# Kernel tuning notes

Measured on AMD Instinct MI355X. Metric: run time of the kernel, lower is better.

The kernel has to match this reference:

```python
import jax, jax.numpy as jnp
import numpy as np

H = 2  # attention heads (n_heads)


def _time_enc(t, tw, tb):
    # TGN TimeEncode: cos(t * w + b); t [...,] -> [..., T]
    return jnp.cos(t[..., None] * tw + tb)


def _level0(nodes, node_features, memory_tab):
    # memory[src] + node_features[src]
    return memory_tab[nodes] + node_features[nodes]


def _aggregate(l, src_feat, src_te, neigh, ete, efeat, mask,
               Wq, bq, Wk, bk, Wv, bv, Wo, bo, fc1_w, fc1_b, fc2_w, fc2_b):
    # Temporal graph attention (TGN TemporalAttentionLayer) with padding mask.
    N, K, _ = neigh.shape
    Dq = Wq.shape[-1]
    dh = Dq // H
    q_in = jnp.concatenate([src_feat[:, None, :], src_te], axis=-1)   # [N,1,Dq]
    k_in = jnp.concatenate([neigh, ete, efeat], axis=-1)              # [N,K,Dk]
    q = (q_in @ Wq[l] + bq[l]).reshape(N, 1, H, dh)
    k = (k_in @ Wk[l] + bk[l]).reshape(N, K, H, dh)
    v = (k_in @ Wv[l] + bv[l]).reshape(N, K, H, dh)
    scores = jnp.einsum('nqhd,nkhd->nhqk', q, k) / jnp.sqrt(jnp.asarray(dh, q.dtype))
    all_masked = mask.all(axis=-1)                                    # [N]
    # TGN trick: un-mask column 0 for fully-masked rows, zero output later
    eff_mask = mask & ~(all_masked[:, None] & (jnp.arange(K) == 0))
    scores = jnp.where(eff_mask[:, None, None, :], -1e9, scores)
    attn = jax.nn.softmax(scores, axis=-1)
    o = jnp.einsum('nhqk,nkhd->nqhd', attn, v).reshape(N, Dq)
    o = o @ Wo[l] + bo[l]
    o = jnp.where(all_masked[:, None], 0.0, o)
    # MergeLayer: fc2(relu(fc1(cat[attn_out, src_feat])))
    h = jax.nn.relu(jnp.concatenate([o, src_feat], axis=-1) @ fc1_w[l] + fc1_b[l])
    return h @ fc2_w[l] + fc2_b[l]


def setup_inputs() -> dict:
    key = jax.random.key(0)
    ks = jax.random.split(key, 24)
    B, K, Nn, Ne, D, T = 2048, 20, 1_000_000, 1_000_000, 128, 128
    Dq, Dk = D + T, D + T + D
    inp = {}
    inp['node_features'] = jax.random.normal(ks[0], (Nn, D), jnp.float32) * 0.1
    inp['edge_feat_table'] = jax.random.normal(ks[1], (Ne, D), jnp.float32) * 0.1
    inp['memory_tab'] = jax.random.normal(ks[2], (Nn, D), jnp.float32) * 0.1
    inp['timestamps'] = jax.random.uniform(ks[3], (B,), jnp.float32) * 100.0
    inp['etimes_src'] = jax.random.uniform(ks[4], (B, K), jnp.float32) * 100.0
    inp['etimes_nbr'] = jax.random.uniform(ks[5], (B * K, K), jnp.float32) * 100.0
    inp['tw'] = jax.random.normal(ks[6], (T,), jnp.float32)
    inp['tb'] = jax.random.normal(ks[7], (T,), jnp.float32)
    inp['Wq'] = jax.random.normal(ks[8], (2, Dq, Dq), jnp.float32) / np.sqrt(Dq)
    inp['bq'] = jnp.zeros((2, Dq), jnp.float32)
    inp['Wk'] = jax.random.normal(ks[9], (2, Dk, Dq), jnp.float32) / np.sqrt(Dk)
    inp['bk'] = jnp.zeros((2, Dq), jnp.float32)
    inp['Wv'] = jax.random.normal(ks[10], (2, Dk, Dq), jnp.float32) / np.sqrt(Dk)
    inp['bv'] = jnp.zeros((2, Dq), jnp.float32)
    inp['Wo'] = jax.random.normal(ks[11], (2, Dq, Dq), jnp.float32) / np.sqrt(Dq)
    inp['bo'] = jnp.zeros((2, Dq), jnp.float32)
    inp['fc1_w'] = jax.random.normal(ks[12], (2, Dq + D, D), jnp.float32) / np.sqrt(Dq + D)
    inp['fc1_b'] = jnp.zeros((2, D), jnp.float32)
    inp['fc2_w'] = jax.random.normal(ks[13], (2, D, D), jnp.float32) / np.sqrt(D)
    inp['fc2_b'] = jnp.zeros((2, D), jnp.float32)
    inp['source_nodes'] = jax.random.randint(ks[14], (B,), 0, Nn)
    inp['nbrs_src'] = jax.random.randint(ks[15], (B, K), 0, Nn)
    inp['eidx_src'] = jax.random.randint(ks[16], (B, K), 0, Ne)
    inp['nbrs_nbr'] = jax.random.randint(ks[17], (B * K, K), 0, Nn)
    inp['eidx_nbr'] = jax.random.randint(ks[18], (B * K, K), 0, Ne)
    return inp


def reference(node_features, edge_feat_table, memory_tab, timestamps,
              etimes_src, etimes_nbr, tw, tb,
              Wq, bq, Wk, bk, Wv, bv, Wo, bo, fc1_w, fc1_b, fc2_w, fc2_b,
              source_nodes, nbrs_src, eidx_src, nbrs_nbr, eidx_nbr):
    B, K = nbrs_src.shape
    D = node_features.shape[-1]
    params = (Wq, bq, Wk, bk, Wv, bv, Wo, bo, fc1_w, fc1_b, fc2_w, fc2_b)

    def layer1(nodes, ts, nbrs, eidx, etimes):
        # one temporal-attention hop (n_layers == 1 recursion level)
        src = _level0(nodes, node_features, memory_tab)                 # [N,D]
        neigh = _level0(nbrs.reshape(-1), node_features, memory_tab).reshape(*nbrs.shape, D)
        ete = _time_enc(ts[:, None] - etimes, tw, tb)                   # [N,K,T]
        src_te = _time_enc(jnp.zeros((nodes.shape[0], 1), ts.dtype), tw, tb)
        efeat = edge_feat_table[eidx]                                   # [N,K,De]
        mask = nbrs == 0
        return _aggregate(0, src, src_te, neigh, ete, efeat, mask, *params)

    # layer-1 embedding of sources (recursion uses same temporal neighbors)
    src_conv = layer1(source_nodes, timestamps, nbrs_src, eidx_src, etimes_src)  # [B,D]
    # layer-1 embedding of the sources' neighbors
    ts_rep = jnp.repeat(timestamps, K)                                  # [B*K]
    neigh_emb = layer1(nbrs_src.reshape(-1), ts_rep, nbrs_nbr, eidx_nbr, etimes_nbr)
    neigh_emb = neigh_emb.reshape(B, K, D)
    # layer-2 aggregation over the sources' neighbors
    ete = _time_enc(timestamps[:, None] - etimes_src, tw, tb)           # [B,K,T]
    src_te = _time_enc(jnp.zeros((B, 1), timestamps.dtype), tw, tb)
    efeat = edge_feat_table[eidx_src]
    mask = nbrs_src == 0
    return _aggregate(1, src_conv, src_te, neigh_emb, ete, efeat, mask, *params)
```

## Files before the change

kernel.cpp:

```cpp
#include <hip/hip_runtime.h>
#include <hip/hip_bf16.h>

#define NB   2048
#define KN   20
#define DF   128
#define DQ   256
#define DKI  384
#define NR1  43008
#define SCALE 0.08838834764831845f

typedef short s16x8 __attribute__((ext_vector_type(8)));
typedef short s16x4 __attribute__((ext_vector_type(4)));
typedef float f32x4 __attribute__((ext_vector_type(4)));

__device__ __hip_bfloat16 g_S   [(size_t)NR1*128];
__device__ __hip_bfloat16 g_QKH [(size_t)NR1*768];
__device__ __hip_bfloat16 g_CTX [(size_t)NR1*768];
__device__ __hip_bfloat16 g_Ob  [(size_t)NR1*256];
__device__ __hip_bfloat16 g_FC1A[(size_t)NR1*384];
__device__ float          g_out1[(size_t)NR1*DF];
__device__ float          g_Wqk [2*256*768];
__device__ float          g_bqk [2*768];
__device__ float          g_bqkv[2*768];
__device__ unsigned char  g_allm[NR1];
__device__ __hip_bfloat16 g_Bqk[2*98304];
__device__ __hip_bfloat16 g_Bv [4*49152];
__device__ __hip_bfloat16 g_Bo [2*65536];
__device__ __hip_bfloat16 g_B1 [2*49152];
__device__ __hip_bfloat16 g_B2 [2*16384];

__device__ __forceinline__ short f2bf(float v) {
  union { __hip_bfloat16 h; short s; } u; u.h = __float2bfloat16(v); return u.s;
}
__device__ __forceinline__ float2 bfpair(unsigned u) {
  union { unsigned u2; float f; } a, b;
  a.u2 = u << 16;
  b.u2 = u & 0xFFFF0000u;
  float2 r; r.x = a.f; r.y = b.f; return r;
}
__device__ __forceinline__ s16x4 pack4(float x, float y, float z, float w) {
  s16x4 o; o[0]=f2bf(x); o[1]=f2bf(y); o[2]=f2bf(z); o[3]=f2bf(w); return o;
}
__device__ __forceinline__ unsigned packbf2(float2 v) {
  return (unsigned)(unsigned short)f2bf(v.x) | ((unsigned)(unsigned short)f2bf(v.y) << 16);
}

__global__ __launch_bounds__(256)
void k_wprep1(const float* __restrict__ Wq, const float* __restrict__ Wk,
              const float* __restrict__ bq, const float* __restrict__ Wv,
              const float* __restrict__ Wo, const float* __restrict__ f1w,
              const float* __restrict__ f2w) {
  int b = blockIdx.x;
  if (b < 1536) {
    int idx = b*256 + threadIdx.x;
    int L = idx / 196608, rem = idx % 196608;
    int n = rem >> 8, co = rem & 255;
    int h = n / 384, i = n - h*384;
    const float* wqp = Wq + (size_t)L*DQ*DQ  + (size_t)co*DQ + h*128;
    const float* wkp = Wk + (size_t)L*DKI*DQ + (size_t)i*DQ  + h*128;
    float acc = 0.f;
    #pragma unroll 4
    for (int c = 0; c < 128; ++c) acc += wqp[c]*wkp[c];
    g_Wqk[(size_t)(L*256 + co)*768 + n] = acc;
    if (co == 0) {
      const float* bqp = bq + L*DQ + h*128;
      float bb = 0.f;
      for (int c = 0; c < 128; ++c) bb += bqp[c]*wkp[c];
      g_bqk[L*768 + n] = bb;
    }
    return;
  }
  b -= 1536;
  const float* src; int ldsrc, K, N; __hip_bfloat16* dst;
  if (b < 96)       { int j = b/24; int L=j>>1, h=j&1;
                      src = Wv + (size_t)L*DKI*DQ + h*128; ldsrc=256; K=384; N=128;
                      dst = g_Bv + (size_t)j*49152; b %= 24; }
  else if (b < 160) { b -= 96; int L = b/32;
                      src = Wo + (size_t)L*DQ*DQ; ldsrc=256; K=256; N=256;
                      dst = g_Bo + (size_t)L*65536; b %= 32; }
  else if (b < 208) { b -= 160; int L = b/24;
                      src = f1w + (size_t)L*384*128; ldsrc=128; K=384; N=128;
                      dst = g_B1 + (size_t)L*49152; b %= 24; }
  else              { b -= 208; int L = b/8;
                      src = f2w + (size_t)L*128*128; ldsrc=128; K=128; N=128;
                      dst = g_B2 + (size_t)L*16384; b %= 8; }
  int slot = b*256 + threadIdx.x;
  if (slot >= (K*N)/8) return;
  int cl = slot & 15, t = slot >> 4;
  int kgn = K >> 3;
  int kg = t % kgn, nt = t / kgn;
  int n = nt*16 + cl;
  s16x8 o;
  #pragma unroll
  for (int e = 0; e < 8; ++e) o[e] = f2bf(src[(size_t)(kg*8 + e)*ldsrc + n]);
  *(s16x8*)(dst + (size_t)slot*8) = o;
}

__global__ __launch_bounds__(256)
void k_wprep2(const float* __restrict__ tb) {
  int b = blockIdx.x;
  if (b < 96) {
    int L = b / 48;
    int slot = (b % 48)*256 + threadIdx.x;
    int cl = slot & 15, t = slot >> 4;
    int kg = t & 15, nt = t >> 4;
    int n = nt*16 + cl;
    s16x8 o;
    #pragma unroll
    for (int e = 0; e < 8; ++e)
      o[e] = f2bf(g_Wqk[(size_t)(L*256 + kg*8 + e)*768 + n] * SCALE);
    *(s16x8*)(g_Bqk + (size_t)L*98304 + (size_t)slot*8) = o;
  } else {
    int idx = (b - 96)*256 + threadIdx.x;
    int L = idx / 768, n = idx % 768;
    float acc = g_bqk[idx];
    for (int c = 0; c < 128; ++c)
      acc += cosf(tb[c]) * g_Wqk[(size_t)(L*256 + 128 + c)*768 + n];
    g_bqkv[idx] = acc * SCALE;
  }
}

template<int L>
__global__ __launch_bounds__(256)
void k_prep(const float* __restrict__ nf, const float* __restrict__ mem,
            const int* __restrict__ srcn, const int* __restrict__ nbs) {
  const int tid = threadIdx.x;
  const int rl = tid >> 5, q = tid & 31, d0 = q*4;
  const int r = blockIdx.x*8 + rl;
  float ax, ay, az, aw;
  if (L == 0) {
    int node = (r < NB) ? srcn[r] : nbs[r - NB];
    float4 x = *(const float4*)(mem + (size_t)node*DF + d0);
    float4 y = *(const float4*)(nf  + (size_t)node*DF + d0);
    ax=x.x+y.x; ay=x.y+y.y; az=x.z+y.z; aw=x.w+y.w;
  } else {
    float4 x = *(const float4*)(g_out1 + (size_t)r*DF + d0);
    ax=x.x; ay=x.y; az=x.z; aw=x.w;
  }
  s16x4 p = pack4(ax, ay, az, aw);
  *(s16x4*)(g_S + (size_t)r*128 + d0) = p;
  *(s16x4*)(g_FC1A + (size_t)r*384 + 256 + d0) = p;
}

template<int L>
__global__ __launch_bounds__(256, 4)
void k_edge(const float* __restrict__ nf, const float* __restrict__ ef,
            const float* __restrict__ mem, const float* __restrict__ tsv,
            const float* __restrict__ ets, const float* __restrict__ etn,
            const float* __restrict__ tw,  const float* __restrict__ tb,
            const int* __restrict__ nbs, const int* __restrict__ eis,
            const int* __restrict__ nbn, const int* __restrict__ ein,
            const __hip_bfloat16* __restrict__ QKH,
            __hip_bfloat16* __restrict__ CTX)
{
  const int tid = threadIdx.x;
  const int lane = tid & 63, w = tid >> 6;
  const int r = blockIdx.x*4 + w;

  int raw_ = 1, nd_ = 0, ei_ = 0; float dt_ = 0.f;
  if (lane < KN) {
    if (L == 0) {
      if (r < NB) { raw_ = nbs[r*KN+lane]; nd_ = raw_; ei_ = eis[r*KN+lane]; dt_ = tsv[r] - ets[r*KN+lane]; }
      else { int mm = (r-NB)*KN + lane; raw_ = nbn[mm]; nd_ = raw_; ei_ = ein[mm]; dt_ = tsv[(r-NB)/KN] - etn[mm]; }
    } else {
      raw_ = nbs[r*KN+lane]; nd_ = NB + r*KN + lane; ei_ = eis[r*KN+lane]; dt_ = tsv[r] - ets[r*KN+lane];
    }
  }
  unsigned long long bal = __ballot(lane < KN && raw_ == 0);
  unsigned mb = (unsigned)(bal & 0xFFFFFull);
  if (lane == 0) g_allm[r] = (mb == 0xFFFFFu) ? 1 : 0;

  const __hip_bfloat16* Qr = QKH + (size_t)r*768;
  float2 q0[3], q1[3];
  #pragma unroll
  for (int seg = 0; seg < 3; ++seg) {
    q0[seg] = bfpair(*(const unsigned*)(Qr +       seg*128 + 2*lane));
    q1[seg] = bfpair(*(const unsigned*)(Qr + 384 + seg*128 + 2*lane));
  }
  float2 twr = *(const float2*)(tw + 2*lane);
  float2 tbr = *(const float2*)(tb + 2*lane);

  float m0 = -3.0e38f, m1 = -3.0e38f;
  float su0 = 0.f, su1 = 0.f;
  float2 c0n = {0,0}, c0t = {0,0}, c0e = {0,0};
  float2 c1n = {0,0}, c1t = {0,0}, c1e = {0,0};

  #pragma unroll
  for (int c0i = 0; c0i < KN; c0i += 5) {
    int nds[5], eir[5]; float dtr[5];
    #pragma unroll
    for (int e = 0; e < 5; ++e) {
      nds[e] = __shfl(nd_, c0i + e);
      eir[e] = __shfl(ei_, c0i + e);
      dtr[e] = __shfl(dt_, c0i + e);
    }
    float2 vm[5], vf[5], vef[5];
    #pragma unroll
    for (int e = 0; e < 5; ++e) {
      if (L == 0) {
        vm[e] = *(const float2*)(mem + (size_t)nds[e]*DF + 2*lane);
        vf[e] = *(const float2*)(nf  + (size_t)nds[e]*DF + 2*lane);
      } else {
        vm[e] = *(const float2*)(g_out1 + (size_t)nds[e]*DF + 2*lane);
      }
      vef[e] = *(const float2*)(ef + (size_t)eir[e]*DF + 2*lane);
    }
    #pragma unroll
    for (int e = 0; e < 5; ++e) {
      float2 vn;
      if (L == 0) { vn.x = vm[e].x + vf[e].x; vn.y = vm[e].y + vf[e].y; }
      else        vn = vm[e];
      float2 vt;
      vt.x = __cosf(dtr[e]*twr.x + tbr.x);
      vt.y = __cosf(dtr[e]*twr.y + tbr.y);
      float p0 = vn.x*q0[0].x + vn.y*q0[0].y + vt.x*q0[1].x + vt.y*q0[1].y
               + vef[e].x*q0[2].x + vef[e].y*q0[2].y;
      float p1 = vn.x*q1[0].x + vn.y*q1[0].y + vt.x*q1[1].x + vt.y*q1[1].y
               + vef[e].x*q1[2].x + vef[e].y*q1[2].y;
      #pragma unroll
      for (int off = 1; off < 64; off <<= 1) {
        p0 += __shfl_xor(p0, off);
        p1 += __shfl_xor(p1, off);
      }
      const bool msk = (mb >> (c0i + e)) & 1u;
      float s0 = msk ? -1e9f : p0;
      float s1 = msk ? -1e9f : p1;
      if (s0 > m0) {
        float f = __expf(m0 - s0);
        su0 *= f;
        c0n.x *= f; c0n.y *= f; c0t.x *= f; c0t.y *= f; c0e.x *= f; c0e.y *= f;
        m0 = s0;
      }
      float w0 = __expf(s0 - m0);
      su0 += w0;
      c0n.x += w0*vn.x;    c0n.y += w0*vn.y;
      c0t.x += w0*vt.x;    c0t.y += w0*vt.y;
      c0e.x += w0*vef[e].x; c0e.y += w0*vef[e].y;
      if (s1 > m1) {
        float f = __expf(m1 - s1);
        su1 *= f;
        c1n.x *= f; c1n.y *= f; c1t.x *= f; c1t.y *= f; c1e.x *= f; c1e.y *= f;
        m1 = s1;
      }
      float w1 = __expf(s1 - m1);
      su1 += w1;
      c1n.x += w1*vn.x;    c1n.y += w1*vn.y;
      c1t.x += w1*vt.x;    c1t.y += w1*vt.y;
      c1e.x += w1*vef[e].x; c1e.y += w1*vef[e].y;
    }
  }

  float i0 = 1.f / su0, i1 = 1.f / su1;
  c0n.x *= i0; c0n.y *= i0; c0t.x *= i0; c0t.y *= i0; c0e.x *= i0; c0e.y *= i0;
  c1n.x *= i1; c1n.y *= i1; c1t.x *= i1; c1t.y *= i1; c1e.x *= i1; c1e.y *= i1;
  unsigned* C32 = (unsigned*)(CTX + (size_t)r*768);
  C32[0*64 + lane] = packbf2(c0n);
  C32[1*64 + lane] = packbf2(c0t);
  C32[2*64 + lane] = packbf2(c0e);
  C32[3*64 + lane] = packbf2(c1n);
  C32[4*64 + lane] = packbf2(c1t);
  C32[5*64 + lane] = packbf2(c1e);
}

template<int KT, bool F32OUT, bool RELU, bool MASK>
__global__ __launch_bounds__(256, 2)
void k_gemm(const __hip_bfloat16* __restrict__ A, int lda,
            const __hip_bfloat16* __restrict__ B, int kgtot, int nblk,
            void* __restrict__ Cout, int ldc,
            const float* __restrict__ bias,
            const unsigned char* __restrict__ mask, int acolbn)
{
  __shared__ __hip_bfloat16 As[2][128*40];
  __shared__ __hip_bfloat16 Bs[2][128*32];
  const int tid  = threadIdx.x;
  const int lane = tid & 63, wid = tid >> 6;
  const int wm = wid >> 1, wn = wid & 1;
  const int rl = lane & 15, kgs = lane >> 4;
  const int bm = blockIdx.x / nblk, bn = blockIdx.x % nblk;

  f32x4 acc[4][4];
  #pragma unroll
  for (int i = 0; i < 4; ++i)
    #pragma unroll
    for (int j = 0; j < 4; ++j) acc[i][j] = (f32x4){0.f,0.f,0.f,0.f};

  #define STAGE(T, BUF) {                                                      \
    _Pragma("unroll")                                                          \
    for (int i_ = 0; i_ < 2; ++i_) {                                           \
      int row_ = i_*64 + (tid >> 2), kc_ = (tid & 3)*8;                        \
      s16x8 v_ = *(const s16x8*)(A + (size_t)(bm*128 + row_)*lda + bn*acolbn + (T)*32 + kc_); \
      *(s16x8*)(&As[BUF][row_*40 + kc_]) = v_;                                 \
    }                                                                          \
    _Pragma("unroll")                                                          \
    for (int i_ = 0; i_ < 2; ++i_) {                                           \
      int slot_ = i_*256 + tid;                                                \
      int nt_ = slot_ >> 6, kg_ = (slot_ >> 4) & 3, cl_ = slot_ & 15;          \
      s16x8 w_ = *(const s16x8*)(B + ((size_t)(bn*8 + nt_)*kgtot + (T)*4 + kg_)*128 + cl_*8); \
      *(s16x8*)(&Bs[BUF][slot_*8]) = w_;                                       \
    } }

  STAGE(0, 0);
  __syncthreads();
  int buf = 0;
  for (int t = 0; t < KT; ++t) {
    if (t < KT-1) STAGE(t+1, buf ^ 1);
    s16x8 af[4], bfm[4];
    #pragma unroll
    for (int mtl = 0; mtl < 4; ++mtl)
      af[mtl] = *(const s16x8*)(&As[buf][(wm*64 + mtl*16 + rl)*40 + kgs*8]);
    #pragma unroll
    for (int ntl = 0; ntl < 4; ++ntl)
      bfm[ntl] = *(const s16x8*)(&Bs[buf][((wn*4 + ntl)*4 + kgs)*128 + rl*8]);
    #pragma unroll
    for (int mtl = 0; mtl < 4; ++mtl)
      #pragma unroll
      for (int ntl = 0; ntl < 4; ++ntl)
        acc[mtl][ntl] = __builtin_amdgcn_mfma_f32_16x16x32_bf16(af[mtl], bfm[ntl], acc[mtl][ntl], 0, 0, 0);
    __syncthreads();
    buf ^= 1;
  }
  #undef STAGE

  #pragma unroll
  for (int mtl = 0; mtl < 4; ++mtl) {
    #pragma unroll
    for (int ntl = 0; ntl < 4; ++ntl) {
      int gcol = bn*128 + wn*64 + ntl*16 + rl;
      float bb = bias ? bias[gcol] : 0.f;
      #pragma unroll
      for (int rg = 0; rg < 4; ++rg) {
        int grow = bm*128 + wm*64 + mtl*16 + kgs*4 + rg;
        float v = acc[mtl][ntl][rg] + bb;
        if (RELU) v = fmaxf(v, 0.f);
        if (MASK) { if (mask[grow]) v = 0.f; }
        if (F32OUT) ((float*)Cout)[(size_t)grow*ldc + gcol] = v;
        else ((__hip_bfloat16*)Cout)[(size_t)grow*ldc + gcol] = __float2bfloat16(v);
      }
    }
  }
}

__global__ __launch_bounds__(256, 2)
void k_mlp(const __hip_bfloat16* __restrict__ A,
           const __hip_bfloat16* __restrict__ B1t,
           const __hip_bfloat16* __restrict__ B2t,
           const float* __restrict__ b1, const float* __restrict__ b2,
           float* __restrict__ Cout)
{
  __shared__ __hip_bfloat16 As[2][128*40];
  __shared__ __hip_bfloat16 Bs[2][128*32];
  __shared__ __hip_bfloat16 Hb[128*136];
  const int tid  = threadIdx.x;
  const int lane = tid & 63, wid = tid >> 6;
  const int wm = wid >> 1, wn = wid & 1;
  const int rl = lane & 15, kgs = lane >> 4;
  const int bm = blockIdx.x;

  f32x4 acc[4][4];
  #pragma unroll
  for (int i = 0; i < 4; ++i)
    #pragma unroll
    for (int j = 0; j < 4; ++j) acc[i][j] = (f32x4){0.f,0.f,0.f,0.f};

  #define STAGE1(T, BUF) {                                                     \
    _Pragma("unroll")                                                          \
    for (int i_ = 0; i_ < 2; ++i_) {                                           \
      int row_ = i_*64 + (tid >> 2), kc_ = (tid & 3)*8;                        \
      s16x8 v_ = *(const s16x8*)(A + (size_t)(bm*128 + row_)*384 + (T)*32 + kc_); \
      *(s16x8*)(&As[BUF][row_*40 + kc_]) = v_;                                 \
    }                                                                          \
    _Pragma("unroll")                                                          \
    for (int i_ = 0; i_ < 2; ++i_) {                                           \
      int slot_ = i_*256 + tid;                                                \
      int nt_ = slot_ >> 6, kg_ = (slot_ >> 4) & 3, cl_ = slot_ & 15;          \
      s16x8 w_ = *(const s16x8*)(B1t + ((size_t)nt_*48 + (T)*4 + kg_)*128 + cl_*8); \
      *(s16x8*)(&Bs[BUF][slot_*8]) = w_;                                       \
    } }

  STAGE1(0, 0);
  __syncthreads();
  int buf = 0;
  for (int t = 0; t < 12; ++t) {
    if (t < 11) STAGE1(t+1, buf ^ 1);
    s16x8 af[4], bfm[4];
    #pragma unroll
    for (int mtl = 0; mtl < 4; ++mtl)
      af[mtl] = *(const s16x8*)(&As[buf][(wm*64 + mtl*16 + rl)*40 + kgs*8]);
    #pragma unroll
    for (int ntl = 0; ntl < 4; ++ntl)
      bfm[ntl] = *(const s16x8*)(&Bs[buf][((wn*4 + ntl)*4 + kgs)*128 + rl*8]);
    #pragma unroll
    for (int mtl = 0; mtl < 4; ++mtl)
      #pragma unroll
      for (int ntl = 0; ntl < 4; ++ntl)
        acc[mtl][ntl] = __builtin_amdgcn_mfma_f32_16x16x32_bf16(af[mtl], bfm[ntl], acc[mtl][ntl], 0, 0, 0);
    __syncthreads();
    buf ^= 1;
  }
  #undef STAGE1

  #pragma unroll
  for (int mtl = 0; mtl < 4; ++mtl) {
    #pragma unroll
    for (int ntl = 0; ntl < 4; ++ntl) {
      int col = wn*64 + ntl*16 + rl;
      float bb = b1[col];
      #pragma unroll
      for (int rg = 0; rg < 4; ++rg) {
        int row = wm*64 + mtl*16 + kgs*4 + rg;
        union { __hip_bfloat16 h; short s; } u;
        u.s = f2bf(fmaxf(acc[mtl][ntl][rg] + bb, 0.f));
        Hb[row*136 + col] = u.h;
      }
    }
  }

  f32x4 acc2[4][4];
  #pragma unroll
  for (int i = 0; i < 4; ++i)
    #pragma unroll
    for (int j = 0; j < 4; ++j) acc2[i][j] = (f32x4){0.f,0.f,0.f,0.f};

  #define STAGE2(T, BUF) {                                                     \
    _Pragma("unroll")                                                          \
    for (int i_ = 0; i_ < 2; ++i_) {                                           \
      int slot_ = i_*256 + tid;                                                \
      int nt_ = slot_ >> 6, kg_ = (slot_ >> 4) & 3, cl_ = slot_ & 15;          \
      s16x8 w_ = *(const s16x8*)(B2t + ((size_t)nt_*16 + (T)*4 + kg_)*128 + cl_*8); \
      *(s16x8*)(&Bs[BUF][slot_*8]) = w_;                                       \
    } }

  STAGE2(0, 0);
  __syncthreads();
  buf = 0;
  for (int t = 0; t < 4; ++t) {
    if (t < 3) STAGE2(t+1, buf ^ 1);
    s16x8 af[4], bfm[4];
    #pragma unroll
    for (int mtl = 0; mtl < 4; ++mtl)
      af[mtl] = *(const s16x8*)(&Hb[(wm*64 + mtl*16 + rl)*136 + t*32 + kgs*8]);
    #pragma unroll
    for (int ntl = 0; ntl < 4; ++ntl)
      bfm[ntl] = *(const s16x8*)(&Bs[buf][((wn*4 + ntl)*4 + kgs)*128 + rl*8]);
    #pragma unroll
    for (int mtl = 0; mtl < 4; ++mtl)
      #pragma unroll
      for (int ntl = 0; ntl < 4; ++ntl)
        acc2[mtl][ntl] = __builtin_amdgcn_mfma_f32_16x16x32_bf16(af[mtl], bfm[ntl], acc2[mtl][ntl], 0, 0, 0);
    __syncthreads();
    buf ^= 1;
  }
  #undef STAGE2

  #pragma unroll
  for (int mtl = 0; mtl < 4; ++mtl) {
    #pragma unroll
    for (int ntl = 0; ntl < 4; ++ntl) {
      int gcol = wn*64 + ntl*16 + rl;
      float bb = b2[gcol];
      #pragma unroll
      for (int rg = 0; rg < 4; ++rg) {
        int grow = bm*128 + wm*64 + mtl*16 + kgs*4 + rg;
        Cout[(size_t)grow*128 + gcol] = acc2[mtl][ntl][rg] + bb;
      }
    }
  }
}

extern "C" void kernel_launch(void* const* d_in, const int* in_sizes, int n_in,
                              void* d_out, int out_size, void* d_ws, size_t ws_size,
                              hipStream_t stream) {
  (void)in_sizes; (void)n_in; (void)out_size; (void)ws_size; (void)d_ws;
  const float* nf   = (const float*)d_in[0];
  const float* ef   = (const float*)d_in[1];
  const float* mem  = (const float*)d_in[2];
  const float* tsv  = (const float*)d_in[3];
  const float* ets  = (const float*)d_in[4];
  const float* etn  = (const float*)d_in[5];
  const float* tw   = (const float*)d_in[6];
  const float* tb   = (const float*)d_in[7];
  const float* Wq   = (const float*)d_in[8];
  const float* bq   = (const float*)d_in[9];
  const float* Wk   = (const float*)d_in[10];
  const float* bv   = (const float*)d_in[13];
  const float* Wv   = (const float*)d_in[12];
  const float* Wo   = (const float*)d_in[14];
  const float* bo   = (const float*)d_in[15];
  const float* f1w  = (const float*)d_in[16];
  const float* f1b  = (const float*)d_in[17];
  const float* f2w  = (const float*)d_in[18];
  const float* f2b  = (const float*)d_in[19];
  const int* srcn   = (const int*)d_in[20];
  const int* nbs    = (const int*)d_in[21];
  const int* eis    = (const int*)d_in[22];
  const int* nbn    = (const int*)d_in[23];
  const int* ein    = (const int*)d_in[24];
  float* out = (float*)d_out;

  __hip_bfloat16 *S, *QKH, *CTX, *Ob, *FC1A, *Bqk, *Bv, *Bo, *B1, *B2;
  float *bqkv, *out1f;
  unsigned char* allm;
  hipGetSymbolAddress((void**)&S,    HIP_SYMBOL(g_S));
  hipGetSymbolAddress((void**)&QKH,  HIP_SYMBOL(g_QKH));
  hipGetSymbolAddress((void**)&CTX,  HIP_SYMBOL(g_CTX));
  hipGetSymbolAddress((void**)&Ob,   HIP_SYMBOL(g_Ob));
  hipGetSymbolAddress((void**)&FC1A, HIP_SYMBOL(g_FC1A));
  hipGetSymbolAddress((void**)&Bqk,  HIP_SYMBOL(g_Bqk));
  hipGetSymbolAddress((void**)&Bv,   HIP_SYMBOL(g_Bv));
  hipGetSymbolAddress((void**)&Bo,   HIP_SYMBOL(g_Bo));
  hipGetSymbolAddress((void**)&B1,   HIP_SYMBOL(g_B1));
  hipGetSymbolAddress((void**)&B2,   HIP_SYMBOL(g_B2));
  hipGetSymbolAddress((void**)&bqkv, HIP_SYMBOL(g_bqkv));
  hipGetSymbolAddress((void**)&out1f,HIP_SYMBOL(g_out1));
  hipGetSymbolAddress((void**)&allm, HIP_SYMBOL(g_allm));

  hipLaunchKernelGGL(k_wprep1, dim3(1760), dim3(256), 0, stream, Wq, Wk, bq, Wv, Wo, f1w, f2w);
  hipLaunchKernelGGL(k_wprep2, dim3(102), dim3(256), 0, stream, tb);

  {
    const int R = NR1, BMg = R/128;
    hipLaunchKernelGGL((k_prep<0>), dim3(R/8), dim3(256), 0, stream, nf, mem, srcn, nbs);
    hipLaunchKernelGGL((k_gemm<4,false,false,false>), dim3(BMg*6), dim3(256), 0, stream,
        S, 128, Bqk, 16, 6, QKH, 768, bqkv, (const unsigned char*)nullptr, 0);
    hipLaunchKernelGGL((k_edge<0>), dim3(R/4), dim3(256), 0, stream,
        nf, ef, mem, tsv, ets, etn, tw, tb, nbs, eis, nbn, ein, QKH, CTX);
    hipLaunchKernelGGL((k_gemm<12,false,false,false>), dim3(BMg*2), dim3(256), 0, stream,
        CTX, 768, Bv, 48, 2, Ob, 256, bv, (const unsigned char*)nullptr, 384);
    hipLaunchKernelGGL((k_gemm<8,false,false,true>), dim3(BMg*2), dim3(256), 0, stream,
        Ob, 256, Bo, 32, 2, FC1A, 384, bo, allm, 0);
    hipLaunchKernelGGL(k_mlp, dim3(BMg), dim3(256), 0, stream,
        FC1A, B1, B2, f1b, f2b, out1f);
  }
  {
    const int R = NB, BMg = R/128;
    hipLaunchKernelGGL((k_prep<1>), dim3(R/8), dim3(256), 0, stream, nf, mem, srcn, nbs);
    hipLaunchKernelGGL((k_gemm<4,false,false,false>), dim3(BMg*6), dim3(256), 0, stream,
        S, 128, Bqk + 98304, 16, 6, QKH, 768, bqkv + 768, (const unsigned char*)nullptr, 0);
    hipLaunchKernelGGL((k_edge<1>), dim3(R/4), dim3(256), 0, stream,
        nf, ef, mem, tsv, ets, etn, tw, tb, nbs, eis, nbn, ein, QKH, CTX);
    hipLaunchKernelGGL((k_gemm<12,false,false,false>), dim3(BMg*2), dim3(256), 0, stream,
        CTX, 768, Bv + 2*49152, 48, 2, Ob, 256, bv + 256, (const unsigned char*)nullptr, 384);
    hipLaunchKernelGGL((k_gemm<8,false,false,true>), dim3(BMg*2), dim3(256), 0, stream,
        Ob, 256, Bo + 65536, 32, 2, FC1A, 384, bo + 256, allm, 0);
    hipLaunchKernelGGL(k_mlp, dim3(BMg), dim3(256), 0, stream,
        FC1A, B1 + 49152, B2 + 16384, f1b + 128, f2b + 128, out);
  }
}
```

Baseline: 556.9 us.

## Fold value and output projections into one precomputed weight

```diff
diff --git a/kernel.cpp b/kernel.cpp
--- a/kernel.cpp
+++ b/kernel.cpp
@@ -16,16 +16,15 @@
 __device__ __hip_bfloat16 g_S   [(size_t)NR1*128];
 __device__ __hip_bfloat16 g_QKH [(size_t)NR1*768];
 __device__ __hip_bfloat16 g_CTX [(size_t)NR1*768];
-__device__ __hip_bfloat16 g_Ob  [(size_t)NR1*256];
 __device__ __hip_bfloat16 g_FC1A[(size_t)NR1*384];
 __device__ float          g_out1[(size_t)NR1*DF];
 __device__ float          g_Wqk [2*256*768];
 __device__ float          g_bqk [2*768];
 __device__ float          g_bqkv[2*768];
+__device__ float          g_bvo [2*256];
 __device__ unsigned char  g_allm[NR1];
 __device__ __hip_bfloat16 g_Bqk[2*98304];
-__device__ __hip_bfloat16 g_Bv [4*49152];
-__device__ __hip_bfloat16 g_Bo [2*65536];
+__device__ __hip_bfloat16 g_Bvo[2*196608];
 __device__ __hip_bfloat16 g_B1 [2*49152];
 __device__ __hip_bfloat16 g_B2 [2*16384];
 
@@ -47,8 +46,7 @@
 
 __global__ __launch_bounds__(256)
 void k_wprep1(const float* __restrict__ Wq, const float* __restrict__ Wk,
-              const float* __restrict__ bq, const float* __restrict__ Wv,
-              const float* __restrict__ Wo, const float* __restrict__ f1w,
+              const float* __restrict__ bq, const float* __restrict__ f1w,
               const float* __restrict__ f2w) {
   int b = blockIdx.x;
   if (b < 1536) {
@@ -72,18 +70,12 @@
   }
   b -= 1536;
   const float* src; int ldsrc, K, N; __hip_bfloat16* dst;
-  if (b < 96)       { int j = b/24; int L=j>>1, h=j&1;
-                      src = Wv + (size_t)L*DKI*DQ + h*128; ldsrc=256; K=384; N=128;
-                      dst = g_Bv + (size_t)j*49152; b %= 24; }
-  else if (b < 160) { b -= 96; int L = b/32;
-                      src = Wo + (size_t)L*DQ*DQ; ldsrc=256; K=256; N=256;
-                      dst = g_Bo + (size_t)L*65536; b %= 32; }
-  else if (b < 208) { b -= 160; int L = b/24;
-                      src = f1w + (size_t)L*384*128; ldsrc=128; K=384; N=128;
-                      dst = g_B1 + (size_t)L*49152; b %= 24; }
-  else              { b -= 208; int L = b/8;
-                      src = f2w + (size_t)L*128*128; ldsrc=128; K=128; N=128;
-                      dst = g_B2 + (size_t)L*16384; b %= 8; }
+  if (b < 48) { int L = b/24;
+                src = f1w + (size_t)L*384*128; ldsrc=128; K=384; N=128;
+                dst = g_B1 + (size_t)L*49152; b %= 24; }
+  else        { b -= 48; int L = b/8;
+                src = f2w + (size_t)L*128*128; ldsrc=128; K=128; N=128;
+                dst = g_B2 + (size_t)L*16384; b %= 8; }
   int slot = b*256 + threadIdx.x;
   if (slot >= (K*N)/8) return;
   int cl = slot & 15, t = slot >> 4;
@@ -117,6 +109,40 @@
     for (int c = 0; c < 128; ++c)
       acc += cosf(tb[c]) * g_Wqk[(size_t)(L*256 + 128 + c)*768 + n];
     g_bqkv[idx] = acc * SCALE;
+  }
+}
+
+__global__ __launch_bounds__(256)
+void k_wprep3(const float* __restrict__ Wv, const float* __restrict__ Wo,
+              const float* __restrict__ bv, const float* __restrict__ bo) {
+  int b = blockIdx.x;
+  if (b < 192) {
+    int idx = b*256 + threadIdx.x;
+    int L = idx / 24576, slot = idx % 24576;
+    int cl = slot & 15, t = slot >> 4;
+    int kg = t % 96, nt = t / 96;
+    int n = nt*16 + cl;
+    int hk = (kg >= 48);
+    const float* wo = Wo + (size_t)L*DQ*DQ + (size_t)(hk*128)*DQ + n;
+    s16x8 o;
+    #pragma unroll
+    for (int e = 0; e < 8; ++e) {
+      int i = (kg - hk*48)*8 + e;
+      const float* wv = Wv + (size_t)L*DKI*DQ + (size_t)i*DQ + hk*128;
+      float acc = 0.f;
+      #pragma unroll 4
+      for (int d = 0; d < 128; ++d) acc += wv[d] * wo[(size_t)d*DQ];
+      o[e] = f2bf(acc);
+    }
+    *(s16x8*)(g_Bvo + (size_t)L*196608 + (size_t)slot*8) = o;
+  } else {
+    int idx = (b - 192)*256 + threadIdx.x;
+    if (idx >= 512) return;
+    int L = idx / 256, n = idx % 256;
+    float acc = bo[L*DQ + n];
+    for (int c = 0; c < 256; ++c)
+      acc += bv[L*DQ + c] * Wo[(size_t)L*DQ*DQ + (size_t)c*DQ + n];
+    g_bvo[idx] = acc;
   }
 }
 
@@ -268,7 +294,7 @@
             const __hip_bfloat16* __restrict__ B, int kgtot, int nblk,
             void* __restrict__ Cout, int ldc,
             const float* __restrict__ bias,
-            const unsigned char* __restrict__ mask, int acolbn)
+            const unsigned char* __restrict__ mask)
 {
   __shared__ __hip_bfloat16 As[2][128*40];
   __shared__ __hip_bfloat16 Bs[2][128*32];
@@ -288,7 +314,7 @@
     _Pragma("unroll")                                                          \
     for (int i_ = 0; i_ < 2; ++i_) {                                           \
       int row_ = i_*64 + (tid >> 2), kc_ = (tid & 3)*8;                        \
-      s16x8 v_ = *(const s16x8*)(A + (size_t)(bm*128 + row_)*lda + bn*acolbn + (T)*32 + kc_); \
+      s16x8 v_ = *(const s16x8*)(A + (size_t)(bm*128 + row_)*lda + (T)*32 + kc_); \
       *(s16x8*)(&As[BUF][row_*40 + kc_]) = v_;                                 \
     }                                                                          \
     _Pragma("unroll")                                                          \
@@ -497,37 +523,35 @@
   const int* ein    = (const int*)d_in[24];
   float* out = (float*)d_out;
 
-  __hip_bfloat16 *S, *QKH, *CTX, *Ob, *FC1A, *Bqk, *Bv, *Bo, *B1, *B2;
-  float *bqkv, *out1f;
+  __hip_bfloat16 *S, *QKH, *CTX, *FC1A, *Bqk, *Bvo, *B1, *B2;
+  float *bqkv, *bvo, *out1f;
   unsigned char* allm;
   hipGetSymbolAddress((void**)&S,    HIP_SYMBOL(g_S));
   hipGetSymbolAddress((void**)&QKH,  HIP_SYMBOL(g_QKH));
   hipGetSymbolAddress((void**)&CTX,  HIP_SYMBOL(g_CTX));
-  hipGetSymbolAddress((void**)&Ob,   HIP_SYMBOL(g_Ob));
   hipGetSymbolAddress((void**)&FC1A, HIP_SYMBOL(g_FC1A));
   hipGetSymbolAddress((void**)&Bqk,  HIP_SYMBOL(g_Bqk));
-  hipGetSymbolAddress((void**)&Bv,   HIP_SYMBOL(g_Bv));
-  hipGetSymbolAddress((void**)&Bo,   HIP_SYMBOL(g_Bo));
+  hipGetSymbolAddress((void**)&Bvo,  HIP_SYMBOL(g_Bvo));
   hipGetSymbolAddress((void**)&B1,   HIP_SYMBOL(g_B1));
   hipGetSymbolAddress((void**)&B2,   HIP_SYMBOL(g_B2));
   hipGetSymbolAddress((void**)&bqkv, HIP_SYMBOL(g_bqkv));
+  hipGetSymbolAddress((void**)&bvo,  HIP_SYMBOL(g_bvo));
   hipGetSymbolAddress((void**)&out1f,HIP_SYMBOL(g_out1));
   hipGetSymbolAddress((void**)&allm, HIP_SYMBOL(g_allm));
 
-  hipLaunchKernelGGL(k_wprep1, dim3(1760), dim3(256), 0, stream, Wq, Wk, bq, Wv, Wo, f1w, f2w);
+  hipLaunchKernelGGL(k_wprep1, dim3(1600), dim3(256), 0, stream, Wq, Wk, bq, f1w, f2w);
   hipLaunchKernelGGL(k_wprep2, dim3(102), dim3(256), 0, stream, tb);
+  hipLaunchKernelGGL(k_wprep3, dim3(194), dim3(256), 0, stream, Wv, Wo, bv, bo);
 
   {
     const int R = NR1, BMg = R/128;
     hipLaunchKernelGGL((k_prep<0>), dim3(R/8), dim3(256), 0, stream, nf, mem, srcn, nbs);
     hipLaunchKernelGGL((k_gemm<4,false,false,false>), dim3(BMg*6), dim3(256), 0, stream,
-        S, 128, Bqk, 16, 6, QKH, 768, bqkv, (const unsigned char*)nullptr, 0);
+        S, 128, Bqk, 16, 6, QKH, 768, bqkv, (const unsigned char*)nullptr);
     hipLaunchKernelGGL((k_edge<0>), dim3(R/4), dim3(256), 0, stream,
         nf, ef, mem, tsv, ets, etn, tw, tb, nbs, eis, nbn, ein, QKH, CTX);
-    hipLaunchKernelGGL((k_gemm<12,false,false,false>), dim3(BMg*2), dim3(256), 0, stream,
-        CTX, 768, Bv, 48, 2, Ob, 256, bv, (const unsigned char*)nullptr, 384);
-    hipLaunchKernelGGL((k_gemm<8,false,false,true>), dim3(BMg*2), dim3(256), 0, stream,
-        Ob, 256, Bo, 32, 2, FC1A, 384, bo, allm, 0);
+    hipLaunchKernelGGL((k_gemm<24,false,false,true>), dim3(BMg*2), dim3(256), 0, stream,
+        CTX, 768, Bvo, 96, 2, FC1A, 384, bvo, allm);
     hipLaunchKernelGGL(k_mlp, dim3(BMg), dim3(256), 0, stream,
         FC1A, B1, B2, f1b, f2b, out1f);
   }
@@ -535,13 +559,11 @@
     const int R = NB, BMg = R/128;
     hipLaunchKernelGGL((k_prep<1>), dim3(R/8), dim3(256), 0, stream, nf, mem, srcn, nbs);
     hipLaunchKernelGGL((k_gemm<4,false,false,false>), dim3(BMg*6), dim3(256), 0, stream,
-        S, 128, Bqk + 98304, 16, 6, QKH, 768, bqkv + 768, (const unsigned char*)nullptr, 0);
+        S, 128, Bqk + 98304, 16, 6, QKH, 768, bqkv + 768, (const unsigned char*)nullptr);
     hipLaunchKernelGGL((k_edge<1>), dim3(R/4), dim3(256), 0, stream,
         nf, ef, mem, tsv, ets, etn, tw, tb, nbs, eis, nbn, ein, QKH, CTX);
-    hipLaunchKernelGGL((k_gemm<12,false,false,false>), dim3(BMg*2), dim3(256), 0, stream,
-        CTX, 768, Bv + 2*49152, 48, 2, Ob, 256, bv + 256, (const unsigned char*)nullptr, 384);
-    hipLaunchKernelGGL((k_gemm<8,false,false,true>), dim3(BMg*2), dim3(256), 0, stream,
-        Ob, 256, Bo + 65536, 32, 2, FC1A, 384, bo + 256, allm, 0);
+    hipLaunchKernelGGL((k_gemm<24,false,false,true>), dim3(BMg*2), dim3(256), 0, stream,
+        CTX, 768, Bvo + 196608, 96, 2, FC1A, 384, bvo + 256, allm);
     hipLaunchKernelGGL(k_mlp, dim3(BMg), dim3(256), 0, stream,
         FC1A, B1 + 49152, B2 + 16384, f1b + 128, f2b + 128, out);
   }
```

New measurement: 591.6 us. 1.06x slower.
